# Performance work log

Hardware: AMD Instinct MI355X
Metric: run time of the kernel (lower is better)

## Reference

```python
import jax, jax.numpy as jnp
import numpy as np


def _conv3x3(x, w, b):
    # x: [B,C,H,W], w: [O,C,3,3]
    y = jax.lax.conv_general_dilated(x, w, window_strides=(1, 1), padding=((1, 1), (1, 1)),
                                     dimension_numbers=('NCHW', 'OIHW', 'NCHW'))
    return y + b[None, :, None, None]


def _radial_weights(ck, wide):
    # ck: [B, wide, H, W] = |radial core|. Returns softmax-normalized per-pixel
    # kernel weights [B, K*K, H, W] with K = 2*wide - 1 (radially symmetric,
    # linearly interpolated between integer radii, zero outside radius mid).
    mid = wide - 1
    ii, jj = np.meshgrid(np.arange(wide), np.arange(wide), indexing='ij')
    d = np.sqrt((ii - mid) ** 2 + (jj - mid) ** 2)
    low = np.floor(d)
    high = np.ceil(d)
    lo_i = np.clip(low, 0, wide - 1).astype(np.int32)
    hi_i = np.clip(high, 0, wide - 1).astype(np.int32)
    mask = (d <= mid).astype(np.float32)  # strictly-greater-than-mid entries zeroed
    w_hi = ((d - low).astype(np.float32)) * mask
    # torch special-cases low==high -> y_low with weight 1
    w_lo = (np.where(low == high, 1.0, high - d).astype(np.float32)) * mask
    w_lo = jnp.asarray(w_lo)[None, :, :, None, None]
    w_hi = jnp.asarray(w_hi)[None, :, :, None, None]
    quad = w_lo * ck[:, lo_i] + w_hi * ck[:, hi_i]  # [B, wide, wide, H, W]
    # flipcat along both spatial kernel dims -> full K x K symmetric kernel
    sym = np.concatenate([np.arange(wide), np.arange(wide - 2, -1, -1)])
    full = quad[:, sym][:, :, sym]  # [B, K, K, H, W]
    B, K, _, H, W = full.shape
    return jax.nn.softmax(full.reshape(B, K * K, H, W), axis=1)


def _kpn_forward(data_with_est, data, w_first, b_first, w_blk1, b_blk1, w_blk2, b_blk2, w_out, b_out):
    x = _conv3x3(data_with_est, w_first, b_first)
    for i in range(3):  # three ResidualBlock_noBN
        y = jax.nn.relu(_conv3x3(x, w_blk1[i], b_blk1[i]))
        x = x + _conv3x3(y, w_blk2[i], b_blk2[i])
    core = _conv3x3(x, w_out, b_out)  # [B, 35, H, W]

    B, N, H, W = data.shape
    outs = [data]
    off = 0
    for wide in range(2, 9):  # sections [2,3,4,5,6,7,8] -> K in 3,5,...,15
        K = 2 * wide - 1
        ck = jnp.abs(core[:, off:off + wide])
        off += wide
        wts = _radial_weights(ck, wide)  # [B, K*K, H, W]
        r = K // 2
        fp = jnp.pad(data, ((0, 0), (0, 0), (r, r), (r, r)))
        # unfold: K*K shifted views, stacked on a new axis -> [B, N, K*K, H, W]
        stack = jnp.stack([fp[:, :, i:i + H, j:j + W]
                           for i in range(K) for j in range(K)], axis=2)
        pred = jnp.sum(wts[:, None] * stack, axis=2)  # [B, N, H, W]
        outs.append(pred)
    return tuple(outs)


def setup_inputs() -> dict:
    key = jax.random.key(0)
    ks = jax.random.split(key, 8)
    B, N, H, W = 1, 3, 384, 384
    f = lambda k, s: jax.random.normal(k, s, dtype=jnp.float32) * 0.05
    return {
        'data_with_est': jax.random.normal(ks[0], (B, 6, H, W), dtype=jnp.float32),
        'data': jax.random.normal(ks[1], (B, N, H, W), dtype=jnp.float32),
        'w_first': f(ks[2], (64, 6, 3, 3)),
        'b_first': jnp.zeros((64,), jnp.float32),
        'w_blk1': f(ks[3], (3, 64, 64, 3, 3)),
        'b_blk1': jnp.zeros((3, 64), jnp.float32),
        'w_blk2': f(ks[4], (3, 64, 64, 3, 3)),
        'b_blk2': jnp.zeros((3, 64), jnp.float32),
        'w_out': f(ks[5], (35, 64, 3, 3)),
        'b_out': jnp.zeros((35,), jnp.float32),
    }


def reference(data_with_est, data, w_first, b_first, w_blk1, b_blk1, w_blk2, b_blk2, w_out, b_out):
    return _kpn_forward(data_with_est, data, w_first, b_first, w_blk1, b_blk1,
                        w_blk2, b_blk2, w_out, b_out)
```

## Files before the change

kernel.cpp:

```cpp
#include <hip/hip_runtime.h>
#include <hip/hip_bf16.h>
#include <utility>

typedef __attribute__((ext_vector_type(4))) float f32x4;
typedef float f32x4u __attribute__((ext_vector_type(4), aligned(4)));
typedef __attribute__((ext_vector_type(8))) short bf16x8;
typedef __attribute__((ext_vector_type(4))) unsigned short u16x4;
typedef unsigned short u16;

constexpr int HH = 384, WW = 384;
constexpr int AWP = 386;
constexpr int ASTR = AWP * 64;
constexpr int NPIX = HH * WW;
constexpr int NPIX3 = NPIX * 3;
constexpr int DP = 398, DPLANE = DP * DP;
constexpr size_t ACT_BYTES = (size_t)AWP * AWP * 64 * 2;
constexpr int WSW = 72 * 512;
constexpr int WP1N = 12 * 512;

__device__ __forceinline__ u16 f2bf(float f) {
  union { __hip_bfloat16 h; u16 u; } v; v.h = __float2bfloat16(f); return v.u;
}
__device__ __forceinline__ float bf2f(u16 u) {
  union { float f; unsigned int i; } v; v.i = ((unsigned int)u) << 16; return v.f;
}

constexpr int PR_REPACK = 7 * WSW + 448 + WP1N;
constexpr int PR_PADCOPY = PR_REPACK + NPIX3;
constexpr int PR_PAD6 = PR_PADCOPY + NPIX;
constexpr int PR_HALO = PR_PAD6 + 49280 + 3080 + 32844;

__global__ void prep_kern(const float* __restrict__ w1, const float* __restrict__ w2,
                          const float* __restrict__ wo, const float* __restrict__ b1,
                          const float* __restrict__ b2, const float* __restrict__ bo,
                          const float* __restrict__ wf, const float* __restrict__ data,
                          const float* __restrict__ din6,
                          u16* __restrict__ wpack, float* __restrict__ bpack,
                          u16* __restrict__ wp1, float* __restrict__ dpad,
                          u16* __restrict__ in8, u16* __restrict__ A0,
                          u16* __restrict__ A1)
{
  const int gidx = blockIdx.x * 256 + threadIdx.x;
  if (gidx < PR_REPACK) {
    const int idx = gidx;
    constexpr int NW = 7 * WSW;
    if (idx < NW) {
      const int c = idx / WSW;
      const int r = idx % WSW;
      const int iter = r / 512;
      const int lane = (r % 512) / 8;
      const int j = r % 8;
      const int tap = iter >> 3;
      const int ich = (iter >> 2) & 1;
      const int m = iter & 3;
      const int oc = m * 16 + (lane & 15);
      const int ic = ich * 32 + (lane >> 4) * 8 + j;
      float v;
      if (c < 6) {
        const float* s = (c & 1) ? w2 : w1;
        v = s[(((c >> 1) * 64 + oc) * 64 + ic) * 9 + tap];
      } else {
        v = (oc < 35) ? wo[(oc * 64 + ic) * 9 + tap] : 0.f;
      }
      wpack[idx] = f2bf(v);
    } else if (idx < NW + 448) {
      const int t = idx - NW;
      const int c = t / 64, oc = t % 64;
      float v;
      if (c < 6) v = ((c & 1) ? b2 : b1)[(c >> 1) * 64 + oc];
      else v = (oc < 35) ? bo[oc] : 0.f;
      bpack[t] = v;
    } else {
      const int t = idx - NW - 448;
      const int iter = t / 512;
      const int lane = (t % 512) / 8;
      const int j = t % 8;
      const int m = iter & 3;
      const int kb = iter >> 2;
      const int oc = m * 16 + (lane & 15);
      const int k = kb * 32 + (lane >> 4) * 8 + j;
      const int tap = k >> 3, ic = k & 7;
      const float v = (tap < 9 && ic < 6) ? wf[oc * 54 + ic * 9 + tap] : 0.f;
      wp1[t] = f2bf(v);
    }
  } else if (gidx < PR_PADCOPY) {
    const int idx = gidx - PR_REPACK;
    const int c = idx / NPIX, r = idx % NPIX;
    const int y = r / WW, x = r % WW;
    dpad[c * DPLANE + (y + 7) * DP + (x + 7)] = data[idx];
  } else if (gidx < PR_PAD6) {
    const int px = gidx - PR_PADCOPY;
    const int y = px / WW, x = px % WW;
    u16 vals[8];
    #pragma unroll
    for (int ic = 0; ic < 6; ++ic) vals[ic] = f2bf(din6[ic * NPIX + px]);
    vals[6] = 0; vals[7] = 0;
    u16* o = in8 + ((size_t)(y + 1) * AWP + (x + 1)) * 8;
    *(u16x4*)(o) = u16x4{vals[0], vals[1], vals[2], vals[3]};
    *(u16x4*)(o + 4) = u16x4{vals[4], vals[5], vals[6], vals[7]};
  } else if (gidx < PR_HALO) {
    const int idx = gidx - PR_PAD6;
    if (idx < 49280) {
      u16* buf = (idx < 24640) ? A0 : A1;
      const int t = (idx < 24640) ? idx : idx - 24640;
      const int pos = t >> 4, q = t & 15;
      int y, x;
      if (pos < 386) { y = 0; x = pos; }
      else if (pos < 772) { y = 385; x = pos - 386; }
      else if (pos < 1156) { y = pos - 772 + 1; x = 0; }
      else { y = pos - 1156 + 1; x = 385; }
      *(u16x4*)(buf + ((size_t)y * AWP + x) * 64 + q * 4) = u16x4{0, 0, 0, 0};
    } else if (idx < 49280 + 3080) {
      const int t = idx - 49280;
      const int pos = t >> 1, q = t & 1;
      int y, x;
      if (pos < 386) { y = 0; x = pos; }
      else if (pos < 772) { y = 385; x = pos - 386; }
      else if (pos < 1156) { y = pos - 772 + 1; x = 0; }
      else { y = pos - 1156 + 1; x = 385; }
      *(u16x4*)(in8 + ((size_t)y * AWP + x) * 8 + q * 4) = u16x4{0, 0, 0, 0};
    } else {
      const int t = idx - 52360;
      const int c = t / 10948, r = t % 10948;
      int y, x;
      if (r < 2786) { y = r / 398; x = r % 398; }
      else if (r < 5572) { const int rr = r - 2786; y = 391 + rr / 398; x = rr % 398; }
      else { const int rr = r - 5572; y = 7 + rr / 14; const int k = rr % 14; x = (k < 7) ? k : 384 + k; }
      dpad[(size_t)c * DPLANE + (size_t)y * DP + x] = 0.f;
    }
  }
}

__global__ __launch_bounds__(64)
void conv1_mfma(const u16* __restrict__ in8, const u16* __restrict__ wp,
                const float* __restrict__ bias, u16* __restrict__ outb)
{
  const int lane = threadIdx.x;
  const int l15 = lane & 15, g8 = lane >> 4;
  const int bid = blockIdx.x;
  const int sw = (bid & 7) * 288 + (bid >> 3);
  const int y = sw / 6;
  const int x0 = (sw % 6) * 64;

  f32x4 acc[4][4];
  #pragma unroll
  for (int m = 0; m < 4; ++m)
    #pragma unroll
    for (int n = 0; n < 4; ++n)
      acc[m][n] = f32x4{0.f, 0.f, 0.f, 0.f};

  #pragma unroll
  for (int kb = 0; kb < 3; ++kb) {
    const int tap = kb * 4 + g8;
    const int vt = tap < 9 ? tap : 0;
    const int kr = vt / 3, kc = vt % 3;
    const u16* inr = in8 + ((size_t)(y + kr) * AWP + x0 + kc) * 8;
    bf16x8 a[4], b[4];
    #pragma unroll
    for (int m = 0; m < 4; ++m)
      a[m] = *(const bf16x8*)(wp + (kb * 4 + m) * 512 + lane * 8);
    #pragma unroll
    for (int n = 0; n < 4; ++n)
      b[n] = *(const bf16x8*)(inr + (size_t)(n * 16 + l15) * 8);
    #pragma unroll
    for (int m = 0; m < 4; ++m)
      #pragma unroll
      for (int n = 0; n < 4; ++n)
        acc[m][n] = __builtin_amdgcn_mfma_f32_16x16x32_bf16(a[m], b[n], acc[m][n], 0, 0, 0);
  }

  const int oc_lo = g8 * 4;
  #pragma unroll
  for (int m = 0; m < 4; ++m) {
    const int oc0 = m * 16 + oc_lo;
    const f32x4 bv = *(const f32x4*)(bias + oc0);
    #pragma unroll
    for (int n = 0; n < 4; ++n) {
      const int px = x0 + n * 16 + l15;
      const f32x4 v = acc[m][n] + bv;
      u16x4 s;
      #pragma unroll
      for (int j = 0; j < 4; ++j) s[j] = f2bf(v[j]);
      *(u16x4*)(outb + ((size_t)(y + 1) * AWP + (px + 1)) * 64 + oc0) = s;
    }
  }
}

template<int MODE>
__global__ __launch_bounds__(256, 3)
void conv_mfma(const u16* __restrict__ in, const u16* __restrict__ wp,
               const float* __restrict__ bias, u16* __restrict__ outb,
               float* __restrict__ outf)
{
  constexpr int MM = (MODE == 2) ? 3 : 4;
  __shared__ u16 smem[3 * 136 * 64];
  const int lane = threadIdx.x & 63;
  const int wv = threadIdx.x >> 6;
  const int pxh = wv >> 1;
  const int ich = wv & 1;
  const int l15 = lane & 15, g8 = lane >> 4;
  const int bid = blockIdx.x;
  const int sw = (bid & 7) * 144 + (bid >> 3);
  const int y = sw / 3;
  const int x0 = (sw % 3) * 128;

  {
    const int pxl = lane >> 3;
    const int s = lane & 7;
    #pragma unroll
    for (int row = 0; row < 3; ++row) {
      const char* gbase = (const char*)(in + (size_t)(y + row) * ASTR + (size_t)x0 * 64);
      #pragma unroll
      for (int j = 0; j < 17; ++j) {
        if (((row * 17 + j) & 3) == wv) {
          const int px = j * 8 + pxl;
          const char* g = gbase + px * 128 + ((s ^ (px & 7)) << 4);
          __builtin_amdgcn_global_load_lds(
              (__attribute__((address_space(1))) const void*)g,
              (__attribute__((address_space(3))) void*)((char*)smem + row * 17408 + j * 1024),
              16, 0, 0);
        }
      }
    }
  }
  __syncthreads();

  f32x4 acc[MM][4];
  #pragma unroll
  for (int m = 0; m < MM; ++m)
    #pragma unroll
    for (int n = 0; n < 4; ++n)
      acc[m][n] = f32x4{0.f, 0.f, 0.f, 0.f};

  const int chunk = ich * 4 + g8;
  #pragma unroll
  for (int tap = 0; tap < 9; ++tap) {
    const int kr = tap / 3, kc = tap % 3;
    const u16* wpi = wp + ((tap * 2 + ich) * 4) * 512 + lane * 8;
    bf16x8 a[MM], b[4];
    #pragma unroll
    for (int m = 0; m < MM; ++m)
      a[m] = *(const bf16x8*)(wpi + m * 512);
    #pragma unroll
    for (int n = 0; n < 4; ++n) {
      const int p = pxh * 64 + kc + n * 16 + l15;
      const char* bp = (const char*)smem + kr * 17408 + p * 128 + ((chunk ^ (p & 7)) << 4);
      b[n] = *(const bf16x8*)bp;
    }
    #pragma unroll
    for (int m = 0; m < MM; ++m)
      #pragma unroll
      for (int n = 0; n < 4; ++n)
        acc[m][n] = __builtin_amdgcn_mfma_f32_16x16x32_bf16(a[m], b[n], acc[m][n], 0, 0, 0);
  }

  __syncthreads();
  float* red = (float*)smem;
  if (ich == 1) {
    #pragma unroll
    for (int m = 0; m < MM; ++m)
      #pragma unroll
      for (int n = 0; n < 4; ++n)
        *(f32x4*)(red + pxh * 4096 + (m * 4 + n) * 256 + lane * 4) = acc[m][n];
  }
  __syncthreads();
  if (ich == 1) return;

  const int oc_lo = g8 * 4;
  #pragma unroll
  for (int m = 0; m < MM; ++m) {
    const int oc0 = m * 16 + oc_lo;
    const f32x4 bv = *(const f32x4*)(bias + oc0);
    #pragma unroll
    for (int n = 0; n < 4; ++n) {
      const int px = x0 + pxh * 64 + n * 16 + l15;
      f32x4 v = acc[m][n] + *(const f32x4*)(red + pxh * 4096 + (m * 4 + n) * 256 + lane * 4) + bv;
      if constexpr (MODE == 0) {
        #pragma unroll
        for (int j = 0; j < 4; ++j) v[j] = v[j] > 0.f ? v[j] : 0.f;
      }
      if constexpr (MODE == 1) {
        const u16x4 rr = *(const u16x4*)(outb + ((size_t)(y + 1) * AWP + (px + 1)) * 64 + oc0);
        #pragma unroll
        for (int j = 0; j < 4; ++j) v[j] += bf2f(rr[j]);
      }
      if constexpr (MODE <= 1) {
        u16x4 s;
        #pragma unroll
        for (int j = 0; j < 4; ++j) s[j] = f2bf(v[j]);
        *(u16x4*)(outb + ((size_t)(y + 1) * AWP + (px + 1)) * 64 + oc0) = s;
      } else {
        #pragma unroll
        for (int j = 0; j < 4; ++j) {
          const int oc = oc0 + j;
          if (oc < 35) outf[(size_t)oc * NPIX + (size_t)y * WW + px] = v[j];
        }
      }
    }
  }
}

constexpr int isqrt_(int d2) { int li = 0; while ((li + 1) * (li + 1) <= d2) ++li; return li; }
constexpr double csqrt_(double x) {
  double g = x < 1.0 ? 1.0 : x;
  for (int i = 0; i < 60; ++i) g = 0.5 * (g + x / g);
  return g;
}
constexpr int KOFFS[7] = {0, 2, 5, 9, 14, 20, 27};

template<int SEC0, int NSEC, int CKN, int A, int B, int T>
__device__ __forceinline__ void kpn_sec_one(const float (&g)[3], const float (&ck)[CKN],
                                            float (&s)[NSEC], float (&p)[NSEC][3])
{
  constexpr int WIDE = SEC0 + T + 2;
  if constexpr (A < WIDE && B < WIDE) {
    constexpr int d2 = A * A + B * B;
    constexpr int li = isqrt_(d2);
    constexpr bool exact = (li * li == d2);
    constexpr int hraw = exact ? li : li + 1;
    constexpr float dd = (float)csqrt_((double)d2);
    constexpr float wlo = exact ? 1.0f : ((float)hraw - dd);
    constexpr float whi = exact ? 0.0f : (dd - (float)li);
    constexpr float mult = ((A > 0) ? 2.0f : 1.0f) * ((B > 0) ? 2.0f : 1.0f);
    constexpr int lidx = li < WIDE - 1 ? li : WIDE - 1;
    constexpr int hidx = hraw < WIDE - 1 ? hraw : WIDE - 1;
    constexpr bool msk = d2 <= (WIDE - 1) * (WIDE - 1);
    constexpr int cb = KOFFS[SEC0 + T] - KOFFS[SEC0];
    float e;
    if constexpr (msk) e = __expf(wlo * ck[cb + lidx] + whi * ck[cb + hidx]);
    else e = 1.0f;
    s[T] += mult * e;
    p[T][0] += e * g[0];
    p[T][1] += e * g[1];
    p[T][2] += e * g[2];
  }
}

template<int SEC0, int NSEC, int CKN, int A, int B, int... Ts>
__device__ __forceinline__ void kpn_secs(std::integer_sequence<int, Ts...>,
                                         const float (&g)[3], const float (&ck)[CKN],
                                         float (&s)[NSEC], float (&p)[NSEC][3])
{
  (kpn_sec_one<SEC0, NSEC, CKN, A, B, Ts>(g, ck, s, p), ...);
}

template<int SEC0, int NSEC, int CKN, int A, int B>
__device__ __forceinline__ void kpn_bcol(const float (&rf)[3][8], const float (&ck)[CKN],
                                         float (&s)[NSEC], float (&p)[NSEC][3])
{
  const float g[3] = {rf[0][B], rf[1][B], rf[2][B]};
  kpn_secs<SEC0, NSEC, CKN, A, B>(std::make_integer_sequence<int, NSEC>{}, g, ck, s, p);
}

template<int SEC0, int NSEC, int CKN, int A, int... Bs>
__device__ __forceinline__ void kpn_bcols(std::integer_sequence<int, Bs...>,
                                          const float (&rf)[3][8], const float (&ck)[CKN],
                                          float (&s)[NSEC], float (&p)[NSEC][3])
{
  (kpn_bcol<SEC0, NSEC, CKN, A, Bs>(rf, ck, s, p), ...);
}

template<int SEC0, int NSEC, int CKN, int WMAX, int A>
__device__ __forceinline__ void kpn_arow(const float* __restrict__ base,
                                         const float (&ck)[CKN],
                                         float (&s)[NSEC], float (&p)[NSEC][3])
{
  float rf[3][8];
  #pragma unroll
  for (int c = 0; c < 3; ++c) {
    const float* bc = base + c * DPLANE;
    f32x4u v[4];
    #pragma unroll
    for (int q = 0; q < 4; ++q)
      v[q] = *(const f32x4u*)(bc + A * DP - 7 + q * 4);
    if constexpr (A > 0) {
      #pragma unroll
      for (int q = 0; q < 4; ++q) {
        const f32x4u w = *(const f32x4u*)(bc - A * DP - 7 + q * 4);
        v[q] += w;
      }
    }
    rf[c][0] = v[1][3];
    rf[c][1] = v[2][0] + v[1][2];
    rf[c][2] = v[2][1] + v[1][1];
    rf[c][3] = v[2][2] + v[1][0];
    rf[c][4] = v[2][3] + v[0][3];
    rf[c][5] = v[3][0] + v[0][2];
    rf[c][6] = v[3][1] + v[0][1];
    rf[c][7] = v[3][2] + v[0][0];
  }
  kpn_bcols<SEC0, NSEC, CKN, A>(std::make_integer_sequence<int, WMAX>{}, rf, ck, s, p);
}

template<int SEC0, int NSEC, int CKN, int WMAX, int... As>
__device__ __forceinline__ void kpn_arows(std::integer_sequence<int, As...>,
                                          const float* __restrict__ base,
                                          const float (&ck)[CKN],
                                          float (&s)[NSEC], float (&p)[NSEC][3])
{
  (kpn_arow<SEC0, NSEC, CKN, WMAX, As>(base, ck, s, p), ...);
}

template<int SEC0, int NSEC>
__device__ __forceinline__ void kpn_grp_body(const float* __restrict__ corep,
                                             const float* __restrict__ dpad,
                                             float* __restrict__ out)
{
  constexpr int WMAX = SEC0 + NSEC + 1;
  constexpr int CK0 = KOFFS[SEC0];
  constexpr int CKN = KOFFS[SEC0 + NSEC - 1] + (SEC0 + NSEC + 1) - CK0;

  const int bid = blockIdx.x;
  const int sw = (bid & 7) * 72 + (bid >> 3);
  const int px = sw * 256 + threadIdx.x;
  const int y = px / WW, x = px % WW;
  const float* base = dpad + (size_t)(y + 7) * DP + (x + 7);

  float ck[CKN];
  #pragma unroll
  for (int i = 0; i < CKN; ++i) ck[i] = fabsf(corep[(size_t)(CK0 + i) * NPIX + px]);

  float s[NSEC], p[NSEC][3];
  #pragma unroll
  for (int k = 0; k < NSEC; ++k) { s[k] = 0.f; p[k][0] = 0.f; p[k][1] = 0.f; p[k][2] = 0.f; }

  kpn_arows<SEC0, NSEC, CKN, WMAX>(std::make_integer_sequence<int, WMAX>{},
                                   base, ck, s, p);

  #pragma unroll
  for (int t = 0; t < NSEC; ++t) {
    const float inv = 1.f / s[t];
    float* o = out + (size_t)(SEC0 + t + 1) * NPIX3 + px;
    o[0] = p[t][0] * inv;
    o[NPIX] = p[t][1] * inv;
    o[2 * NPIX] = p[t][2] * inv;
  }
}

__global__ __launch_bounds__(256)
void kpn_fused7(const float* __restrict__ corep, const float* __restrict__ dpad,
                float* __restrict__ out)
{
  kpn_grp_body<0, 7>(corep, dpad, out);
}

extern "C" void kernel_launch(void* const* d_in, const int* in_sizes, int n_in,
                              void* d_out, int out_size, void* d_ws, size_t ws_size,
                              hipStream_t stream)
{
  const float* d_est   = (const float*)d_in[0];
  const float* data    = (const float*)d_in[1];
  const float* w_first = (const float*)d_in[2];
  const float* b_first = (const float*)d_in[3];
  const float* w_blk1  = (const float*)d_in[4];
  const float* b_blk1  = (const float*)d_in[5];
  const float* w_blk2  = (const float*)d_in[6];
  const float* b_blk2  = (const float*)d_in[7];
  const float* w_out   = (const float*)d_in[8];
  const float* b_out   = (const float*)d_in[9];

  char* ws = (char*)d_ws;
  const size_t OFF_A1    = ACT_BYTES;
  const size_t OFF_CORE  = 2 * ACT_BYTES;
  const size_t OFF_DPAD  = OFF_CORE + (size_t)35 * NPIX * 4;
  const size_t OFF_WPACK = OFF_DPAD + (size_t)3 * DPLANE * 4;
  const size_t OFF_BPACK = OFF_WPACK + (size_t)7 * WSW * 2;
  const size_t OFF_WP1   = OFF_BPACK + 448 * 4;
  const size_t OFF_IN8   = OFF_WP1 + (size_t)WP1N * 2;

  u16*   A0    = (u16*)(ws);
  u16*   A1    = (u16*)(ws + OFF_A1);
  float* corep = (float*)(ws + OFF_CORE);
  float* dpad  = (float*)(ws + OFF_DPAD);
  u16*   wpack = (u16*)(ws + OFF_WPACK);
  float* bpack = (float*)(ws + OFF_BPACK);
  u16*   wp1   = (u16*)(ws + OFF_WP1);
  u16*   in8   = (u16*)(ws + OFF_IN8);

  hipMemcpyAsync(d_out, data, (size_t)NPIX3 * 4, hipMemcpyDeviceToDevice, stream);

  prep_kern<<<3671, 256, 0, stream>>>(w_blk1, w_blk2, w_out, b_blk1, b_blk2, b_out,
                                      w_first, data, d_est,
                                      wpack, bpack, wp1, dpad, in8, A0, A1);
  conv1_mfma<<<2304, 64, 0, stream>>>(in8, wp1, b_first, A0);

  for (int i = 0; i < 3; ++i) {
    conv_mfma<0><<<1152, 256, 0, stream>>>(A0, wpack + (size_t)(2 * i) * WSW,
                                           bpack + (2 * i) * 64, A1, nullptr);
    conv_mfma<1><<<1152, 256, 0, stream>>>(A1, wpack + (size_t)(2 * i + 1) * WSW,
                                           bpack + (2 * i + 1) * 64, A0, nullptr);
  }
  conv_mfma<2><<<1152, 256, 0, stream>>>(A0, wpack + (size_t)6 * WSW,
                                         bpack + 6 * 64, nullptr, corep);

  kpn_fused7<<<576, 256, 0, stream>>>(corep, dpad, (float*)d_out);
}
```

Before: 181.9 us.

## Split conv output channels across twice as many waves per block

The residual conv kernel goes from 256 to 512 threads per block. The extra waves split the output-channel dimension, so each wave keeps 2 instead of 4 M-tiles of accumulators and issues half the MFMAs per tap. The LDS tile load is spread across 8 waves and the cross-wave reduction buffer is re-indexed per segment. This cuts register pressure and adds waves for latency hiding, at the cost of each wave re-reading the same B fragments from LDS (doubling LDS reads) and more block-level synchronization.

```diff
diff --git a/kernel.cpp b/kernel.cpp
--- a/kernel.cpp
+++ b/kernel.cpp
@@ -187,7 +187,7 @@
 }
 
 template<int MODE>
-__global__ __launch_bounds__(256, 3)
+__global__ __launch_bounds__(512, 6)
 void conv_mfma(const u16* __restrict__ in, const u16* __restrict__ wp,
                const float* __restrict__ bias, u16* __restrict__ outb,
                float* __restrict__ outf)
@@ -196,8 +196,9 @@
   __shared__ u16 smem[3 * 136 * 64];
   const int lane = threadIdx.x & 63;
   const int wv = threadIdx.x >> 6;
-  const int pxh = wv >> 1;
   const int ich = wv & 1;
+  const int pxh = (wv >> 1) & 1;
+  const int mh = wv >> 2;
   const int l15 = lane & 15, g8 = lane >> 4;
   const int bid = blockIdx.x;
   const int sw = (bid & 7) * 144 + (bid >> 3);
@@ -212,7 +213,7 @@
       const char* gbase = (const char*)(in + (size_t)(y + row) * ASTR + (size_t)x0 * 64);
       #pragma unroll
       for (int j = 0; j < 17; ++j) {
-        if (((row * 17 + j) & 3) == wv) {
+        if (((row * 17 + j) & 7) == wv) {
           const int px = j * 8 + pxl;
           const char* g = gbase + px * 128 + ((s ^ (px & 7)) << 4);
           __builtin_amdgcn_global_load_lds(
@@ -225,9 +226,9 @@
   }
   __syncthreads();
 
-  f32x4 acc[MM][4];
-  #pragma unroll
-  for (int m = 0; m < MM; ++m)
+  f32x4 acc[2][4];
+  #pragma unroll
+  for (int m = 0; m < 2; ++m)
     #pragma unroll
     for (int n = 0; n < 4; ++n)
       acc[m][n] = f32x4{0.f, 0.f, 0.f, 0.f};
@@ -237,10 +238,11 @@
   for (int tap = 0; tap < 9; ++tap) {
     const int kr = tap / 3, kc = tap % 3;
     const u16* wpi = wp + ((tap * 2 + ich) * 4) * 512 + lane * 8;
-    bf16x8 a[MM], b[4];
-    #pragma unroll
-    for (int m = 0; m < MM; ++m)
-      a[m] = *(const bf16x8*)(wpi + m * 512);
+    bf16x8 a[2], b[4];
+    #pragma unroll
+    for (int mm = 0; mm < 2; ++mm)
+      if (mh * 2 + mm < MM)
+        a[mm] = *(const bf16x8*)(wpi + (mh * 2 + mm) * 512);
     #pragma unroll
     for (int n = 0; n < 4; ++n) {
       const int p = pxh * 64 + kc + n * 16 + l15;
@@ -248,52 +250,57 @@
       b[n] = *(const bf16x8*)bp;
     }
     #pragma unroll
-    for (int m = 0; m < MM; ++m)
+    for (int mm = 0; mm < 2; ++mm)
+      if (mh * 2 + mm < MM)
+        #pragma unroll
+        for (int n = 0; n < 4; ++n)
+          acc[mm][n] = __builtin_amdgcn_mfma_f32_16x16x32_bf16(a[mm], b[n], acc[mm][n], 0, 0, 0);
+  }
+
+  __syncthreads();
+  float* red = (float*)smem;
+  const int seg = mh * 2 + pxh;
+  if (ich == 1) {
+    #pragma unroll
+    for (int mm = 0; mm < 2; ++mm)
       #pragma unroll
       for (int n = 0; n < 4; ++n)
-        acc[m][n] = __builtin_amdgcn_mfma_f32_16x16x32_bf16(a[m], b[n], acc[m][n], 0, 0, 0);
-  }
-
-  __syncthreads();
-  float* red = (float*)smem;
-  if (ich == 1) {
-    #pragma unroll
-    for (int m = 0; m < MM; ++m)
-      #pragma unroll
-      for (int n = 0; n < 4; ++n)
-        *(f32x4*)(red + pxh * 4096 + (m * 4 + n) * 256 + lane * 4) = acc[m][n];
+        *(f32x4*)(red + seg * 2048 + (mm * 4 + n) * 256 + lane * 4) = acc[mm][n];
   }
   __syncthreads();
   if (ich == 1) return;
 
   const int oc_lo = g8 * 4;
   #pragma unroll
-  for (int m = 0; m < MM; ++m) {
-    const int oc0 = m * 16 + oc_lo;
-    const f32x4 bv = *(const f32x4*)(bias + oc0);
-    #pragma unroll
-    for (int n = 0; n < 4; ++n) {
-      const int px = x0 + pxh * 64 + n * 16 + l15;
-      f32x4 v = acc[m][n] + *(const f32x4*)(red + pxh * 4096 + (m * 4 + n) * 256 + lane * 4) + bv;
-      if constexpr (MODE == 0) {
-        #pragma unroll
-        for (int j = 0; j < 4; ++j) v[j] = v[j] > 0.f ? v[j] : 0.f;
-      }
-      if constexpr (MODE == 1) {
-        const u16x4 rr = *(const u16x4*)(outb + ((size_t)(y + 1) * AWP + (px + 1)) * 64 + oc0);
-        #pragma unroll
-        for (int j = 0; j < 4; ++j) v[j] += bf2f(rr[j]);
-      }
-      if constexpr (MODE <= 1) {
-        u16x4 s;
-        #pragma unroll
-        for (int j = 0; j < 4; ++j) s[j] = f2bf(v[j]);
-        *(u16x4*)(outb + ((size_t)(y + 1) * AWP + (px + 1)) * 64 + oc0) = s;
-      } else {
-        #pragma unroll
-        for (int j = 0; j < 4; ++j) {
-          const int oc = oc0 + j;
-          if (oc < 35) outf[(size_t)oc * NPIX + (size_t)y * WW + px] = v[j];
+  for (int mm = 0; mm < 2; ++mm) {
+    const int m = mh * 2 + mm;
+    if (m < MM) {
+      const int oc0 = m * 16 + oc_lo;
+      const f32x4 bv = *(const f32x4*)(bias + oc0);
+      #pragma unroll
+      for (int n = 0; n < 4; ++n) {
+        const int px = x0 + pxh * 64 + n * 16 + l15;
+        f32x4 v = acc[mm][n] + *(const f32x4*)(red + seg * 2048 + (mm * 4 + n) * 256 + lane * 4) + bv;
+        if constexpr (MODE == 0) {
+          #pragma unroll
+          for (int j = 0; j < 4; ++j) v[j] = v[j] > 0.f ? v[j] : 0.f;
+        }
+        if constexpr (MODE == 1) {
+          const u16x4 rr = *(const u16x4*)(outb + ((size_t)(y + 1) * AWP + (px + 1)) * 64 + oc0);
+          #pragma unroll
+          for (int j = 0; j < 4; ++j) v[j] += bf2f(rr[j]);
+        }
+        if constexpr (MODE <= 1) {
+          u16x4 s;
+          #pragma unroll
+          for (int j = 0; j < 4; ++j) s[j] = f2bf(v[j]);
+          *(u16x4*)(outb + ((size_t)(y + 1) * AWP + (px + 1)) * 64 + oc0) = s;
+        } else {
+          #pragma unroll
+          for (int j = 0; j < 4; ++j) {
+            const int oc = oc0 + j;
+            if (oc < 35) outf[(size_t)oc * NPIX + (size_t)y * WW + px] = v[j];
+          }
         }
       }
     }
@@ -485,12 +492,12 @@
   conv1_mfma<<<2304, 64, 0, stream>>>(in8, wp1, b_first, A0);
 
   for (int i = 0; i < 3; ++i) {
-    conv_mfma<0><<<1152, 256, 0, stream>>>(A0, wpack + (size_t)(2 * i) * WSW,
+    conv_mfma<0><<<1152, 512, 0, stream>>>(A0, wpack + (size_t)(2 * i) * WSW,
                                            bpack + (2 * i) * 64, A1, nullptr);
-    conv_mfma<1><<<1152, 256, 0, stream>>>(A1, wpack + (size_t)(2 * i + 1) * WSW,
+    conv_mfma<1><<<1152, 512, 0, stream>>>(A1, wpack + (size_t)(2 * i + 1) * WSW,
                                            bpack + (2 * i + 1) * 64, A0, nullptr);
   }
-  conv_mfma<2><<<1152, 256, 0, stream>>>(A0, wpack + (size_t)6 * WSW,
+  conv_mfma<2><<<1152, 512, 0, stream>>>(A0, wpack + (size_t)6 * WSW,
                                          bpack + 6 * 64, nullptr, corep);
 
   kpn_fused7<<<576, 256, 0, stream>>>(corep, dpad, (float*)d_out);
```

New measurement: 198.3 us. 1.09x slower.

## Split KPN row loop across two thread halves with shared-memory reduction

Applied to the files above, without the earlier changes.

The fused KPN filtering kernel now assigns two threads per pixel. One half-block handles even kernel rows and the other handles odd rows. The odd half writes its partial softmax sums and weighted sums to shared memory, and the even half adds them and writes the outputs. This doubles the grid to raise parallelism and shorten each thread's serial chain, at the cost of duplicated ck loads, a block barrier, and shared-memory traffic.

```diff
diff --git a/kernel.cpp b/kernel.cpp
--- a/kernel.cpp
+++ b/kernel.cpp
@@ -365,83 +365,98 @@
                                          const float (&ck)[CKN],
                                          float (&s)[NSEC], float (&p)[NSEC][3])
 {
-  float rf[3][8];
-  #pragma unroll
-  for (int c = 0; c < 3; ++c) {
-    const float* bc = base + c * DPLANE;
-    f32x4u v[4];
-    #pragma unroll
-    for (int q = 0; q < 4; ++q)
-      v[q] = *(const f32x4u*)(bc + A * DP - 7 + q * 4);
-    if constexpr (A > 0) {
+  if constexpr (A < WMAX) {
+    float rf[3][8];
+    #pragma unroll
+    for (int c = 0; c < 3; ++c) {
+      const float* bc = base + c * DPLANE;
+      f32x4u v[4];
       #pragma unroll
-      for (int q = 0; q < 4; ++q) {
-        const f32x4u w = *(const f32x4u*)(bc - A * DP - 7 + q * 4);
-        v[q] += w;
+      for (int q = 0; q < 4; ++q)
+        v[q] = *(const f32x4u*)(bc + A * DP - 7 + q * 4);
+      if constexpr (A > 0) {
+        #pragma unroll
+        for (int q = 0; q < 4; ++q) {
+          const f32x4u w = *(const f32x4u*)(bc - A * DP - 7 + q * 4);
+          v[q] += w;
+        }
       }
-    }
-    rf[c][0] = v[1][3];
-    rf[c][1] = v[2][0] + v[1][2];
-    rf[c][2] = v[2][1] + v[1][1];
-    rf[c][3] = v[2][2] + v[1][0];
-    rf[c][4] = v[2][3] + v[0][3];
-    rf[c][5] = v[3][0] + v[0][2];
-    rf[c][6] = v[3][1] + v[0][1];
-    rf[c][7] = v[3][2] + v[0][0];
-  }
-  kpn_bcols<SEC0, NSEC, CKN, A>(std::make_integer_sequence<int, WMAX>{}, rf, ck, s, p);
-}
-
-template<int SEC0, int NSEC, int CKN, int WMAX, int... As>
-__device__ __forceinline__ void kpn_arows(std::integer_sequence<int, As...>,
-                                          const float* __restrict__ base,
-                                          const float (&ck)[CKN],
-                                          float (&s)[NSEC], float (&p)[NSEC][3])
-{
-  (kpn_arow<SEC0, NSEC, CKN, WMAX, As>(base, ck, s, p), ...);
-}
-
-template<int SEC0, int NSEC>
-__device__ __forceinline__ void kpn_grp_body(const float* __restrict__ corep,
-                                             const float* __restrict__ dpad,
-                                             float* __restrict__ out)
-{
-  constexpr int WMAX = SEC0 + NSEC + 1;
-  constexpr int CK0 = KOFFS[SEC0];
-  constexpr int CKN = KOFFS[SEC0 + NSEC - 1] + (SEC0 + NSEC + 1) - CK0;
-
-  const int bid = blockIdx.x;
-  const int sw = (bid & 7) * 72 + (bid >> 3);
-  const int px = sw * 256 + threadIdx.x;
-  const int y = px / WW, x = px % WW;
-  const float* base = dpad + (size_t)(y + 7) * DP + (x + 7);
-
-  float ck[CKN];
-  #pragma unroll
-  for (int i = 0; i < CKN; ++i) ck[i] = fabsf(corep[(size_t)(CK0 + i) * NPIX + px]);
-
-  float s[NSEC], p[NSEC][3];
-  #pragma unroll
-  for (int k = 0; k < NSEC; ++k) { s[k] = 0.f; p[k][0] = 0.f; p[k][1] = 0.f; p[k][2] = 0.f; }
-
-  kpn_arows<SEC0, NSEC, CKN, WMAX>(std::make_integer_sequence<int, WMAX>{},
-                                   base, ck, s, p);
-
-  #pragma unroll
-  for (int t = 0; t < NSEC; ++t) {
-    const float inv = 1.f / s[t];
-    float* o = out + (size_t)(SEC0 + t + 1) * NPIX3 + px;
-    o[0] = p[t][0] * inv;
-    o[NPIX] = p[t][1] * inv;
-    o[2 * NPIX] = p[t][2] * inv;
-  }
+      rf[c][0] = v[1][3];
+      rf[c][1] = v[2][0] + v[1][2];
+      rf[c][2] = v[2][1] + v[1][1];
+      rf[c][3] = v[2][2] + v[1][0];
+      rf[c][4] = v[2][3] + v[0][3];
+      rf[c][5] = v[3][0] + v[0][2];
+      rf[c][6] = v[3][1] + v[0][1];
+      rf[c][7] = v[3][2] + v[0][0];
+    }
+    kpn_bcols<SEC0, NSEC, CKN, A>(std::make_integer_sequence<int, WMAX>{}, rf, ck, s, p);
+  }
+}
+
+template<int SEC0, int NSEC, int CKN, int WMAX, int PAR, int... Is>
+__device__ __forceinline__ void kpn_arows_p(std::integer_sequence<int, Is...>,
+                                            const float* __restrict__ base,
+                                            const float (&ck)[CKN],
+                                            float (&s)[NSEC], float (&p)[NSEC][3])
+{
+  (kpn_arow<SEC0, NSEC, CKN, WMAX, 2 * Is + PAR>(base, ck, s, p), ...);
 }
 
 __global__ __launch_bounds__(256)
 void kpn_fused7(const float* __restrict__ corep, const float* __restrict__ dpad,
                 float* __restrict__ out)
 {
-  kpn_grp_body<0, 7>(corep, dpad, out);
+  constexpr int NSEC = 7, CKN = 35, WMAX = 8;
+  __shared__ float red[128][29];
+  const int bid = blockIdx.x;
+  const int sw = (bid & 7) * 144 + (bid >> 3);
+  const int t = threadIdx.x & 127;
+  const int par = threadIdx.x >> 7;
+  const int px = sw * 128 + t;
+  const int y = px / WW, x = px % WW;
+  const float* base = dpad + (size_t)(y + 7) * DP + (x + 7);
+
+  float ck[CKN];
+  #pragma unroll
+  for (int i = 0; i < CKN; ++i) ck[i] = fabsf(corep[(size_t)i * NPIX + px]);
+
+  float s[NSEC], p[NSEC][3];
+  #pragma unroll
+  for (int k = 0; k < NSEC; ++k) { s[k] = 0.f; p[k][0] = 0.f; p[k][1] = 0.f; p[k][2] = 0.f; }
+
+  if (par == 0)
+    kpn_arows_p<0, NSEC, CKN, WMAX, 0>(std::make_integer_sequence<int, 4>{}, base, ck, s, p);
+  else
+    kpn_arows_p<0, NSEC, CKN, WMAX, 1>(std::make_integer_sequence<int, 4>{}, base, ck, s, p);
+
+  if (par == 1) {
+    #pragma unroll
+    for (int k = 0; k < NSEC; ++k) {
+      red[t][k] = s[k];
+      red[t][7 + k * 3 + 0] = p[k][0];
+      red[t][7 + k * 3 + 1] = p[k][1];
+      red[t][7 + k * 3 + 2] = p[k][2];
+    }
+  }
+  __syncthreads();
+  if (par == 1) return;
+
+  #pragma unroll
+  for (int k = 0; k < NSEC; ++k) {
+    s[k] += red[t][k];
+    p[k][0] += red[t][7 + k * 3 + 0];
+    p[k][1] += red[t][7 + k * 3 + 1];
+    p[k][2] += red[t][7 + k * 3 + 2];
+  }
+  #pragma unroll
+  for (int k = 0; k < NSEC; ++k) {
+    const float inv = 1.f / s[k];
+    float* o = out + (size_t)(k + 1) * NPIX3 + px;
+    o[0] = p[k][0] * inv;
+    o[NPIX] = p[k][1] * inv;
+    o[2 * NPIX] = p[k][2] * inv;
+  }
 }
 
 extern "C" void kernel_launch(void* const* d_in, const int* in_sizes, int n_in,
@@ -493,5 +508,5 @@
   conv_mfma<2><<<1152, 256, 0, stream>>>(A0, wpack + (size_t)6 * WSW,
                                          bpack + 6 * 64, nullptr, corep);
 
-  kpn_fused7<<<576, 256, 0, stream>>>(corep, dpad, (float*)d_out);
-}
+  kpn_fused7<<<1152, 256, 0, stream>>>(corep, dpad, (float*)d_out);
+}
```

Measured after the change: 189.8 us. 4.4% more time.
